# Kernel tuning notes

Hardware: AMD Instinct MI355X
Metric: run time of the kernel (lower is better)

The kernel has to match this reference:

```python
import jax, jax.numpy as jnp
import numpy as np

HID, H, LAT, R = 2048, 16, 512, 32
DH = HID // H          # 128 head_dim
C = DH - R             # 96 content_dim
B, S = 2, 2048


def rotate_half(x):
    h = x.shape[-1] // 2
    return jnp.concatenate([-x[..., h:], x[..., :h]], axis=-1)


def rope_tables(seq_len, dim):
    inv_freq = 1.0 / (10000.0 ** (jnp.arange(0, dim, 2, dtype=jnp.float32) / dim))
    t = jnp.arange(seq_len, dtype=jnp.float32)
    freqs = t[:, None] * inv_freq[None, :]          # [S, dim/2]
    emb = jnp.concatenate([freqs, freqs], axis=-1)  # [S, dim]
    return jnp.cos(emb), jnp.sin(emb)


def setup_inputs() -> dict:
    key = jax.random.key(0)
    ks = jax.random.split(key, 11)
    def lin(k, out_dim, in_dim):
        return jax.random.normal(k, (out_dim, in_dim), jnp.float32) / np.sqrt(in_dim)
    return {
        "x": jax.random.normal(ks[0], (B, S, HID), jnp.float32),
        "Wq_down": lin(ks[1], LAT, HID),
        "Wq_up": lin(ks[2], C * H, LAT),
        "Wq_rope": lin(ks[3], R * H, LAT),
        "Wkv_down": lin(ks[4], LAT, HID),
        "Wk_up": lin(ks[5], C * H, LAT),
        "Wk_rope": lin(ks[6], R, HID),
        "Wv_up": lin(ks[7], HID, LAT),
        "Wo": lin(ks[8], HID, HID),
        "bo": jnp.zeros((HID,), jnp.float32),
    }


def reference(x, Wq_down, Wq_up, Wq_rope, Wkv_down, Wk_up, Wk_rope, Wv_up, Wo, bo):
    Bs, Sl, _ = x.shape
    cos, sin = rope_tables(Sl, R)                       # [S, R]
    cos_b = cos[None, :, None, :]                       # [1,S,1,R]
    sin_b = sin[None, :, None, :]

    # low-rank Q path
    q_lat = jnp.einsum('bsh,lh->bsl', x, Wq_down)       # [B,S,LAT]
    q_c = jnp.einsum('bsl,cl->bsc', q_lat, Wq_up).reshape(Bs, Sl, H, C)
    q_r = jnp.einsum('bsl,rl->bsr', q_lat, Wq_rope).reshape(Bs, Sl, H, R)
    q_r = q_r * cos_b + rotate_half(q_r) * sin_b

    # low-rank KV path
    kv_lat = jnp.einsum('bsh,lh->bsl', x, Wkv_down)     # [B,S,LAT]
    k_c = jnp.einsum('bsl,cl->bsc', kv_lat, Wk_up).reshape(Bs, Sl, H, C)
    k_r = jnp.einsum('bsh,rh->bsr', x, Wk_rope)[:, :, None, :]   # [B,S,1,R]
    k_r = k_r * cos_b + rotate_half(k_r) * sin_b        # [B,S,1,R] (shared per head)
    k_r = jnp.broadcast_to(k_r, (Bs, Sl, H, R))
    v = jnp.einsum('bsl,dl->bsd', kv_lat, Wv_up).reshape(Bs, Sl, H, DH)

    q = jnp.concatenate([q_c, q_r], axis=-1)            # [B,S,H,DH]
    k = jnp.concatenate([k_c, k_r], axis=-1)

    scores = jnp.einsum('bqhd,bkhd->bhqk', q, k) / np.sqrt(DH)
    causal = jnp.triu(jnp.ones((Sl, Sl), bool), k=1)
    scores = jnp.where(causal[None, None], -10000.0, scores)
    attn = jax.nn.softmax(scores, axis=-1)
    ctx = jnp.einsum('bhqk,bkhd->bqhd', attn, v).reshape(Bs, Sl, HID)
    return jnp.einsum('bsd,od->bso', ctx, Wo) + bo
```

## Files before the change

### kernel.cpp

```cpp
#include <hip/hip_runtime.h>
#include <math.h>

#define HIDN 2048
#define NH   16
#define LATN 512
#define RD   32
#define DHD  128
#define CDIM 96
#define NB   2
#define SEQ  2048
#define MTOT 4096

typedef __attribute__((ext_vector_type(8))) short bf8_t;
typedef __attribute__((ext_vector_type(4))) float f4_t;
typedef __attribute__((ext_vector_type(4))) short s4_t;

__device__ __forceinline__ short f2bf(float f) {
    union { float f; unsigned u; } x; x.f = f;
    unsigned r = x.u + 0x7fffu + ((x.u >> 16) & 1u);
    return (short)(r >> 16);
}
__device__ __forceinline__ float bf2f(short s) {
    union { float f; unsigned u; } x; x.u = ((unsigned)(unsigned short)s) << 16;
    return x.f;
}
__device__ __forceinline__ void gload16(const void* g, void* l) {
    __builtin_amdgcn_global_load_lds(
        (const __attribute__((address_space(1))) void*)g,
        (__attribute__((address_space(3))) void*)l, 16, 0, 0);
}

__device__ __forceinline__ float dpp_max16(float x) {
    union { float f; int i; } a, t; a.f = x;
    t.i = __builtin_amdgcn_update_dpp(0, a.i, 0xB1,  0xF, 0xF, true); a.f = fmaxf(a.f, t.f);
    t.i = __builtin_amdgcn_update_dpp(0, a.i, 0x4E,  0xF, 0xF, true); a.f = fmaxf(a.f, t.f);
    t.i = __builtin_amdgcn_update_dpp(0, a.i, 0x124, 0xF, 0xF, true); a.f = fmaxf(a.f, t.f);
    t.i = __builtin_amdgcn_update_dpp(0, a.i, 0x128, 0xF, 0xF, true); a.f = fmaxf(a.f, t.f);
    return a.f;
}
__device__ __forceinline__ float dpp_sum16(float x) {
    union { float f; int i; } a, t; a.f = x;
    t.i = __builtin_amdgcn_update_dpp(0, a.i, 0xB1,  0xF, 0xF, true); a.f += t.f;
    t.i = __builtin_amdgcn_update_dpp(0, a.i, 0x4E,  0xF, 0xF, true); a.f += t.f;
    t.i = __builtin_amdgcn_update_dpp(0, a.i, 0x124, 0xF, 0xF, true); a.f += t.f;
    t.i = __builtin_amdgcn_update_dpp(0, a.i, 0x128, 0xF, 0xF, true); a.f += t.f;
    return a.f;
}

__global__ __launch_bounds__(256)
void cvt_all(const float* __restrict__ x,  const float* __restrict__ w0,
             const float* __restrict__ w1, const float* __restrict__ w2,
             const float* __restrict__ w3, const float* __restrict__ w4,
             const float* __restrict__ w5, const float* __restrict__ w6,
             const float* __restrict__ w7,
             short* xb, short* o0, short* o1, short* o2, short* o3,
             short* o4, short* o5, short* o6, short* o7)
{
    int bid = blockIdx.x;
    const float* src; short* dst; int rel;
    if      (bid < 4096) { src = x;  dst = xb; rel = bid; }
    else if (bid < 4608) { src = w0; dst = o0; rel = bid - 4096; }
    else if (bid < 4992) { src = w1; dst = o1; rel = bid - 4608; }
    else if (bid < 5120) { src = w2; dst = o2; rel = bid - 4992; }
    else if (bid < 5632) { src = w3; dst = o3; rel = bid - 5120; }
    else if (bid < 6016) { src = w4; dst = o4; rel = bid - 5632; }
    else if (bid < 6048) { src = w5; dst = o5; rel = bid - 6016; }
    else if (bid < 6560) { src = w6; dst = o6; rel = bid - 6048; }
    else                 { src = w7; dst = o7; rel = bid - 6560; }
    int base = rel * 2048 + threadIdx.x * 8;
    float4 a = *(const float4*)(src + base);
    float4 b = *(const float4*)(src + base + 4);
    s4_t r0 = { f2bf(a.x), f2bf(a.y), f2bf(a.z), f2bf(a.w) };
    s4_t r1 = { f2bf(b.x), f2bf(b.y), f2bf(b.z), f2bf(b.w) };
    *(s4_t*)(dst + base)     = r0;
    *(s4_t*)(dst + base + 4) = r1;
}

#define EPI_DOWN 0
#define EPI_UP   1
#define EPI_WO   2

template<int KTOT, int EPI>
__global__ __launch_bounds__(256)
void gemm_t(const short* __restrict__ A, const short* __restrict__ W,
            const short* __restrict__ W2,
            void* __restrict__ o1, void* __restrict__ o2,
            void* __restrict__ o3, void* __restrict__ o4,
            const float* __restrict__ bias)
{
    __shared__ short As[2][4096];
    __shared__ short Bs[2][4096];
    const int tid  = threadIdx.x;
    const int w    = tid >> 6;
    const int lane = tid & 63;
    const int l16  = lane & 15;
    const int quad = lane >> 4;
    const int m0 = blockIdx.x * 128;
    int n0 = blockIdx.y * 128;
    const int wm = (w & 1) * 64;
    const int wn = (w >> 1) * 64;

    const short* Ap = A;
    const short* Wp = W;
    int lda, Nrow, job = 0;
    if (EPI == EPI_DOWN) { lda = 2048; Nrow = 1056; }
    if (EPI == EPI_WO)   { lda = 2048; Nrow = 2048; }
    if (EPI == EPI_UP) {
        lda = 1024;
        if (blockIdx.y < 16) { Nrow = 2048; }
        else { job = 1; Ap = A + 512; Wp = W2; n0 = ((int)blockIdx.y - 16) * 128; Nrow = 3584; }
    }

    int srow[2], skc[2], ldso[2];
#pragma unroll
    for (int j = 0; j < 2; ++j) {
        int c = (w * 32 + j * 16) * 4 + lane;
        srow[j] = c >> 2;
        skc[j]  = (c & 3) ^ (srow[j] & 3);
        ldso[j] = (w * 32 + j * 16) * 32;
    }
    const int xq = quad ^ (l16 & 3);

    auto stage = [&](int k0, int buf) {
#pragma unroll
        for (int j = 0; j < 2; ++j) {
            const short* ga = Ap + (size_t)(m0 + srow[j]) * lda + k0 + skc[j] * 8;
            gload16(ga, &As[buf][ldso[j]]);
            int gn = n0 + srow[j]; if (gn >= Nrow) gn = Nrow - 1;
            const short* gb = Wp + (size_t)gn * KTOT + k0 + skc[j] * 8;
            gload16(gb, &Bs[buf][ldso[j]]);
        }
    };

    f4_t acc[4][4];
#pragma unroll
    for (int i = 0; i < 4; ++i)
#pragma unroll
        for (int j = 0; j < 4; ++j) acc[i][j] = (f4_t){0.f, 0.f, 0.f, 0.f};

    stage(0, 0);
    const int nk = KTOT / 32;
    for (int t = 0; t < nk; ++t) {
        const int cur = t & 1;
        __syncthreads();
        if (t + 1 < nk) stage((t + 1) * 32, cur ^ 1);
        bf8_t af[4], bfr[4];
#pragma unroll
        for (int i = 0; i < 4; ++i)
            af[i] = *(const bf8_t*)&As[cur][((wm + i * 16 + l16) * 4 + xq) * 8];
#pragma unroll
        for (int j = 0; j < 4; ++j)
            bfr[j] = *(const bf8_t*)&Bs[cur][((wn + j * 16 + l16) * 4 + xq) * 8];
#pragma unroll
        for (int i = 0; i < 4; ++i)
#pragma unroll
            for (int j = 0; j < 4; ++j)
                acc[i][j] = __builtin_amdgcn_mfma_f32_16x16x32_bf16(
                    af[i], bfr[j], acc[i][j], 0, 0, 0);
    }

#pragma unroll
    for (int mi = 0; mi < 4; ++mi) {
#pragma unroll
        for (int nj = 0; nj < 4; ++nj) {
            const int gm = m0 + wm + mi * 16 + quad * 4;
            const int gn = n0 + wn + nj * 16 + l16;
            const int bb = gm >> 11, ss = gm & 2047;
            if (EPI == EPI_DOWN) {
                if (n0 < 1024) {
                    short* o = (short*)o1 + (size_t)gm * 1024 + gn;
#pragma unroll
                    for (int r = 0; r < 4; ++r) o[(size_t)r * 1024] = f2bf(acc[mi][nj][r]);
                } else if (gn < 1056) {
                    short* o = (short*)o2 + (size_t)gm * 32 + (gn - 1024);
#pragma unroll
                    for (int r = 0; r < 4; ++r) o[(size_t)r * 32] = f2bf(acc[mi][nj][r]);
                }
            } else if (EPI == EPI_WO) {
                float* o = (float*)o1 + (size_t)gm * 2048 + gn;
                float bv = bias[gn];
#pragma unroll
                for (int r = 0; r < 4; ++r) o[(size_t)r * 2048] = acc[mi][nj][r] + bv;
            } else {
                if (job == 0) {
                    if (gn < 1536) {
                        int hh = gn / CDIM, cc = gn % CDIM;
                        short* o = (short*)o1 +
                            (((size_t)(bb * NH + hh) * SEQ + ss) * DHD + cc);
#pragma unroll
                        for (int r = 0; r < 4; ++r) o[(size_t)r * DHD] = f2bf(acc[mi][nj][r]);
                    } else {
                        short* o = (short*)o2 + (size_t)gm * 512 + (gn - 1536);
#pragma unroll
                        for (int r = 0; r < 4; ++r) o[(size_t)r * 512] = f2bf(acc[mi][nj][r]);
                    }
                } else {
                    if (gn < 1536) {
                        int hh = gn / CDIM, cc = gn % CDIM;
                        short* o = (short*)o3 +
                            (((size_t)(bb * NH + hh) * SEQ + ss) * DHD + cc);
#pragma unroll
                        for (int r = 0; r < 4; ++r) o[(size_t)r * DHD] = f2bf(acc[mi][nj][r]);
                    } else {
                        int n2 = gn - 1536;
                        int h2 = n2 >> 7, dh = n2 & 127;
                        size_t idx = ((size_t)(bb * NH + h2) * DHD + dh) * SEQ + ss;
                        s4_t pk = { f2bf(acc[mi][nj][0]), f2bf(acc[mi][nj][1]),
                                    f2bf(acc[mi][nj][2]), f2bf(acc[mi][nj][3]) };
                        *(s4_t*)((short*)o4 + idx) = pk;
                    }
                }
            }
        }
    }
}

__global__ void rope_q_kernel(const short* __restrict__ qr, short* __restrict__ qh)
{
    int idx = blockIdx.x * blockDim.x + threadIdx.x;
    int m = idx >> 9;
    int h = (idx >> 5) & 15;
    int r = idx & 31;
    int b = m >> 11, s = m & (SEQ - 1);
    float invf = expf(-((float)(2 * (r & 15)) / 32.0f) * 9.210340371976184f);
    float f = (float)s * invf;
    float cs = cosf(f), sn = sinf(f);
    float val = bf2f(qr[(size_t)m * 512 + h * 32 + r]);
    float partner = bf2f(qr[(size_t)m * 512 + h * 32 + (r ^ 16)]);
    float rot = (r < 16) ? -partner : partner;
    qh[((size_t)(b * NH + h) * SEQ + s) * DHD + CDIM + r] = f2bf(val * cs + rot * sn);
}

__global__ void rope_k_kernel(const short* __restrict__ kr, short* __restrict__ kh)
{
    int idx = blockIdx.x * blockDim.x + threadIdx.x;
    int m = idx >> 5;
    int r = idx & 31;
    int b = m >> 11, s = m & (SEQ - 1);
    float invf = expf(-((float)(2 * (r & 15)) / 32.0f) * 9.210340371976184f);
    float f = (float)s * invf;
    float cs = cosf(f), sn = sinf(f);
    float val = bf2f(kr[(size_t)m * 32 + r]);
    float partner = bf2f(kr[(size_t)m * 32 + (r ^ 16)]);
    float rot = (r < 16) ? -partner : partner;
    short o = f2bf(val * cs + rot * sn);
    short* dst = kh + ((size_t)b * NH * SEQ + s) * DHD + CDIM + r;
#pragma unroll
    for (int h = 0; h < NH; ++h) dst[(size_t)h * SEQ * DHD] = o;
}

__global__ __launch_bounds__(256)
void attn_mfma(const short* __restrict__ qh, const short* __restrict__ kh,
               const short* __restrict__ vt, short* __restrict__ ctx)
{
    const int h = blockIdx.y, b = blockIdx.z;
    __shared__ short Ks[2][8192];
    __shared__ short Vs[2][8192];
    __shared__ short Ps[4][16][72];
    const int tid  = threadIdx.x;
    const int w    = tid >> 6;
    const int lane = tid & 63;
    const int l16  = lane & 15;
    const int quad = lane >> 4;
    const float qscale = 0.12752956f;

    const short* khead = kh + (size_t)(b * NH + h) * SEQ * DHD;
    const short* vhead = vt + (size_t)(b * NH + h) * DHD * SEQ;

    int koff[4], voff[4], ldso[4];
#pragma unroll
    for (int j = 0; j < 4; ++j) {
        int s = j * 256 + tid;
        int key = s >> 4, c = s & 15;
        koff[j] = key * DHD + (c ^ (key & 15)) * 8;
        int d = s >> 3, c2 = s & 7;
        voff[j] = d * SEQ + (c2 ^ (d & 7)) * 8;
        ldso[j] = (j * 256 + w * 64) * 8;
    }

    for (int phase = 0; phase < 2; ++phase) {
        const int qb = phase ? (31 - (int)blockIdx.x) : (int)blockIdx.x;
        const int q0 = qb * 64;

        bf8_t qf[4];
        {
            const short* qp = qh + ((size_t)(b * NH + h) * SEQ + q0 + w * 16 + l16) * DHD
                                 + quad * 8;
#pragma unroll
            for (int ks = 0; ks < 4; ++ks) {
                bf8_t raw = *(const bf8_t*)(qp + ks * 32);
#pragma unroll
                for (int j = 0; j < 8; ++j) qf[ks][j] = f2bf(bf2f(raw[j]) * qscale);
            }
        }

        f4_t O[8];
#pragma unroll
        for (int i = 0; i < 8; ++i) O[i] = (f4_t){0.f, 0.f, 0.f, 0.f};
        float m_run[4], l_run[4];
#pragma unroll
        for (int r = 0; r < 4; ++r) { m_run[r] = -3e38f; l_run[r] = 0.f; }

        const int ntiles = qb + 1;
        __syncthreads();
#pragma unroll
        for (int j = 0; j < 4; ++j) {
            gload16(khead + koff[j], &Ks[0][ldso[j]]);
            gload16(vhead + voff[j], &Vs[0][ldso[j]]);
        }

        for (int t = 0; t < ntiles; ++t) {
            const int cur = t & 1;
            const int c0 = t * 64;
            __syncthreads();
            if (t + 1 < ntiles) {
                const short* kt = khead + (size_t)(c0 + 64) * DHD;
#pragma unroll
                for (int j = 0; j < 4; ++j) {
                    gload16(kt + koff[j], &Ks[cur ^ 1][ldso[j]]);
                    gload16(vhead + voff[j] + c0 + 64, &Vs[cur ^ 1][ldso[j]]);
                }
            }

            f4_t S[4];
#pragma unroll
            for (int j = 0; j < 4; ++j) S[j] = (f4_t){0.f, 0.f, 0.f, 0.f};
#pragma unroll
            for (int ks = 0; ks < 4; ++ks) {
                const int dch = ks * 4 + quad;
#pragma unroll
                for (int j = 0; j < 4; ++j) {
                    const int slot = (j * 16 + l16) * 16 + (dch ^ l16);
                    bf8_t bj = *(const bf8_t*)&Ks[cur][slot * 8];
                    S[j] = __builtin_amdgcn_mfma_f32_16x16x32_bf16(qf[ks], bj, S[j], 0, 0, 0);
                }
            }

            const int grow0 = q0 + w * 16 + quad * 4;
            float alpha[4];
#pragma unroll
            for (int r = 0; r < 4; ++r) {
                const int grow = grow0 + r;
                float sv[4];
#pragma unroll
                for (int j = 0; j < 4; ++j)
                    sv[j] = (c0 + j * 16 + l16 <= grow) ? S[j][r] : -3e38f;
                float mx = fmaxf(fmaxf(sv[0], sv[1]), fmaxf(sv[2], sv[3]));
                mx = dpp_max16(mx);
                const float mnew = fmaxf(m_run[r], mx);
                alpha[r] = __builtin_amdgcn_exp2f(m_run[r] - mnew);
                float p0 = __builtin_amdgcn_exp2f(sv[0] - mnew);
                float p1 = __builtin_amdgcn_exp2f(sv[1] - mnew);
                float p2 = __builtin_amdgcn_exp2f(sv[2] - mnew);
                float p3 = __builtin_amdgcn_exp2f(sv[3] - mnew);
                float rs = dpp_sum16((p0 + p1) + (p2 + p3));
                l_run[r] = alpha[r] * l_run[r] + rs;
                m_run[r] = mnew;
                short* pr = &Ps[w][quad * 4 + r][l16];
                pr[0]  = f2bf(p0);
                pr[16] = f2bf(p1);
                pr[32] = f2bf(p2);
                pr[48] = f2bf(p3);
            }

#pragma unroll
            for (int dt = 0; dt < 8; ++dt)
#pragma unroll
                for (int r = 0; r < 4; ++r) O[dt][r] *= alpha[r];

#pragma unroll
            for (int ks2 = 0; ks2 < 2; ++ks2) {
                bf8_t pf = *(const bf8_t*)&Ps[w][l16][ks2 * 32 + quad * 8];
#pragma unroll
                for (int dt = 0; dt < 8; ++dt) {
                    const int d = dt * 16 + l16;
                    const int slot = d * 8 + ((ks2 * 4 + quad) ^ (d & 7));
                    bf8_t vf = *(const bf8_t*)&Vs[cur][slot * 8];
                    O[dt] = __builtin_amdgcn_mfma_f32_16x16x32_bf16(pf, vf, O[dt], 0, 0, 0);
                }
            }
        }

        float inv_l[4];
#pragma unroll
        for (int r = 0; r < 4; ++r) inv_l[r] = 1.0f / l_run[r];
        short* cbase = ctx + (size_t)(b * SEQ + q0 + w * 16 + quad * 4) * HIDN
                           + h * DHD + l16;
#pragma unroll
        for (int r = 0; r < 4; ++r)
#pragma unroll
            for (int dt = 0; dt < 8; ++dt)
                cbase[(size_t)r * HIDN + dt * 16] = f2bf(O[dt][r] * inv_l[r]);
    }
}

extern "C" void kernel_launch(void* const* d_in, const int* in_sizes, int n_in,
                              void* d_out, int out_size, void* d_ws, size_t ws_size,
                              hipStream_t stream)
{
    const float* x        = (const float*)d_in[0];
    const float* Wq_down  = (const float*)d_in[1];
    const float* Wq_up    = (const float*)d_in[2];
    const float* Wq_rope  = (const float*)d_in[3];
    const float* Wkv_down = (const float*)d_in[4];
    const float* Wk_up    = (const float*)d_in[5];
    const float* Wk_rope  = (const float*)d_in[6];
    const float* Wv_up    = (const float*)d_in[7];
    const float* Wo       = (const float*)d_in[8];
    const float* bo       = (const float*)d_in[9];
    float* out = (float*)d_out;

    short* ws     = (short*)d_ws;
    short* xb     = ws;
    short* wdownc = ws + 8388608;
    short* wqur   = ws + 10551296;
    short* wkvu   = ws + 11599872;
    short* wob    = ws + 13434880;
    short* qkvlat = ws + 17629184;
    short* qhb    = ws + 21823488;
    short* khb    = ws + 30212096;
    short* vtw    = ws + 38600704;
    short* ctxb   = ws + 46989312;
    short* qrt    = ws + 55377920;
    short* krt    = ws + 57475072;

    dim3 blk(256);
    cvt_all<<<dim3(8608), blk, 0, stream>>>(
        x, Wq_down, Wq_up, Wq_rope, Wkv_down, Wk_up, Wk_rope, Wv_up, Wo,
        xb, wdownc, wqur, wqur + 786432, wdownc + 1048576,
        wkvu, wdownc + 2097152, wkvu + 786432, wob);

    gemm_t<2048, EPI_DOWN><<<dim3(32, 9), blk, 0, stream>>>(
        xb, wdownc, nullptr, qkvlat, krt, nullptr, nullptr, nullptr);
    gemm_t<512, EPI_UP><<<dim3(32, 44), blk, 0, stream>>>(
        qkvlat, wqur, wkvu, qhb, qrt, khb, vtw, nullptr);

    rope_q_kernel<<<dim3(MTOT * NH * RD / 256), blk, 0, stream>>>(qrt, qhb);
    rope_k_kernel<<<dim3(MTOT * RD / 256), blk, 0, stream>>>(krt, khb);

    attn_mfma<<<dim3(16, NH, NB), blk, 0, stream>>>(qhb, khb, vtw, ctxb);

    gemm_t<2048, EPI_WO><<<dim3(32, 16), blk, 0, stream>>>(
        ctxb, wob, nullptr, out, nullptr, nullptr, nullptr, bo);
}
```

Measured before the change: 355.2 us.

## Stage GEMM tiles through registers with two-deep prefetch; skip causal mask off-diagonal

The GEMM main loop stops using direct global-to-LDS loads. It now loads tiles into registers two steps ahead, writes them to the other LDS buffer, and uses a custom barrier that waits only on LDS counters, so global load latency can overlap with MFMA work. The attention kernel applies the causal mask compare only on the diagonal tile and uses raw scores elsewhere. This costs extra VGPRs for the register staging buffers, which may lower occupancy.

Measured after the change: 619.9 us. 74.5% more time.

```diff
diff --git a/kernel.cpp b/kernel.cpp
--- a/kernel.cpp
+++ b/kernel.cpp
@@ -28,6 +28,10 @@
     __builtin_amdgcn_global_load_lds(
         (const __attribute__((address_space(1))) void*)g,
         (__attribute__((address_space(3))) void*)l, 16, 0, 0);
+}
+__device__ __forceinline__ void lds_barrier() {
+    __builtin_amdgcn_s_waitcnt(0xC07F);
+    __builtin_amdgcn_s_barrier();
 }
 
 __device__ __forceinline__ float dpp_max16(float x) {
@@ -117,20 +121,32 @@
         int c = (w * 32 + j * 16) * 4 + lane;
         srow[j] = c >> 2;
         skc[j]  = (c & 3) ^ (srow[j] & 3);
-        ldso[j] = (w * 32 + j * 16) * 32;
+        ldso[j] = c * 8;
     }
     const int xq = quad ^ (l16 & 3);
 
-    auto stage = [&](int k0, int buf) {
+    int4 rA[2][2], rB[2][2];
+    const short* arow[2]; const short* brow[2];
+#pragma unroll
+    for (int j = 0; j < 2; ++j) {
+        arow[j] = Ap + (size_t)(m0 + srow[j]) * lda + skc[j] * 8;
+        int gn = n0 + srow[j]; if (gn >= Nrow) gn = Nrow - 1;
+        brow[j] = Wp + (size_t)gn * KTOT + skc[j] * 8;
+    }
+    auto loadrg = [&](int k0, int st) {
 #pragma unroll
         for (int j = 0; j < 2; ++j) {
-            const short* ga = Ap + (size_t)(m0 + srow[j]) * lda + k0 + skc[j] * 8;
-            gload16(ga, &As[buf][ldso[j]]);
-            int gn = n0 + srow[j]; if (gn >= Nrow) gn = Nrow - 1;
-            const short* gb = Wp + (size_t)gn * KTOT + k0 + skc[j] * 8;
-            gload16(gb, &Bs[buf][ldso[j]]);
+            rA[st][j] = *(const int4*)(arow[j] + k0);
+            rB[st][j] = *(const int4*)(brow[j] + k0);
         }
     };
+    auto wlds = [&](int buf, int st) {
+#pragma unroll
+        for (int j = 0; j < 2; ++j) {
+            *(int4*)&As[buf][ldso[j]] = rA[st][j];
+            *(int4*)&Bs[buf][ldso[j]] = rB[st][j];
+        }
+    };
 
     f4_t acc[4][4];
 #pragma unroll
@@ -138,12 +154,16 @@
 #pragma unroll
         for (int j = 0; j < 4; ++j) acc[i][j] = (f4_t){0.f, 0.f, 0.f, 0.f};
 
-    stage(0, 0);
     const int nk = KTOT / 32;
+    loadrg(0, 0);
+    loadrg(32, 1);
+    wlds(0, 0);
+
     for (int t = 0; t < nk; ++t) {
         const int cur = t & 1;
-        __syncthreads();
-        if (t + 1 < nk) stage((t + 1) * 32, cur ^ 1);
+        lds_barrier();
+        if (t + 1 < nk) wlds(cur ^ 1, (t + 1) & 1);
+        if (t + 2 < nk) loadrg((t + 2) * 32, t & 1);
         bf8_t af[4], bfr[4];
 #pragma unroll
         for (int i = 0; i < 4; ++i)
@@ -337,14 +357,20 @@
             }
 
             const int grow0 = q0 + w * 16 + quad * 4;
+            const bool diag = (t == ntiles - 1);
             float alpha[4];
 #pragma unroll
             for (int r = 0; r < 4; ++r) {
-                const int grow = grow0 + r;
                 float sv[4];
-#pragma unroll
-                for (int j = 0; j < 4; ++j)
-                    sv[j] = (c0 + j * 16 + l16 <= grow) ? S[j][r] : -3e38f;
+                if (diag) {
+                    const int grow = grow0 + r;
+#pragma unroll
+                    for (int j = 0; j < 4; ++j)
+                        sv[j] = (c0 + j * 16 + l16 <= grow) ? S[j][r] : -3e38f;
+                } else {
+#pragma unroll
+                    for (int j = 0; j < 4; ++j) sv[j] = S[j][r];
+                }
                 float mx = fmaxf(fmaxf(sv[0], sv[1]), fmaxf(sv[2], sv[3]));
                 mx = dpp_max16(mx);
                 const float mnew = fmaxf(m_run[r], mx);
```
